# Kernel tuning notes

Measured on AMD Instinct MI355X. Metric: run time of the kernel, lower is better.

The kernel has to match this reference:

```python
import jax, jax.numpy as jnp
import numpy as np

DIM = 1024
NUM_HEADS = 16
HEAD_DIM = DIM // NUM_HEADS


def setup_inputs() -> dict:
    key = jax.random.key(0)
    ks = jax.random.split(key, 8)
    B, N = 4, 1024
    x = jax.random.normal(ks[0], (B, N, DIM), dtype=jnp.float32)
    # RoPE tables per position, broadcast over batch/heads
    pos = jnp.arange(N, dtype=jnp.float32)[:, None]
    inv_freq = 1.0 / (10000.0 ** (jnp.arange(0, HEAD_DIM, 2, dtype=jnp.float32) / HEAD_DIM))
    ang = pos * inv_freq[None, :]                      # [N, D/2]
    ang = jnp.concatenate([ang, ang], axis=-1)          # [N, D]
    cos, sin = jnp.cos(ang), jnp.sin(ang)
    s_in = 1.0 / np.sqrt(DIM)
    qkv_w = jax.random.normal(ks[1], (3 * DIM, DIM), dtype=jnp.float32) * s_in
    qkv_b = jax.random.normal(ks[2], (3 * DIM,), dtype=jnp.float32) * 0.02
    proj_w = jax.random.normal(ks[3], (DIM, DIM), dtype=jnp.float32) * s_in
    proj_b = jax.random.normal(ks[4], (DIM,), dtype=jnp.float32) * 0.02
    return {"x": x, "cos": cos, "sin": sin, "qkv_w": qkv_w, "qkv_b": qkv_b,
            "proj_w": proj_w, "proj_b": proj_b}


def _rotate_half(t):
    t1, t2 = jnp.split(t, 2, axis=-1)
    return jnp.concatenate([-t2, t1], axis=-1)


def reference(x, cos, sin, qkv_w, qkv_b, proj_w, proj_b):
    B, N, C = x.shape
    H, D = NUM_HEADS, HEAD_DIM
    scale = D ** -0.5
    qkv = x @ qkv_w.T + qkv_b                           # [B, N, 3C]
    qkv = qkv.reshape(B, N, 3, H, D).transpose(2, 0, 3, 1, 4)  # [3, B, H, N, D]
    q, k, v = qkv[0], qkv[1], qkv[2]
    q = q * cos + _rotate_half(q) * sin                 # cos/sin [N, D] broadcast
    k = k * cos + _rotate_half(k) * sin
    attn = jnp.einsum('bhnd,bhmd->bhnm', q, k) * scale  # [B, H, N, N]
    attn = jax.nn.softmax(attn, axis=-1)
    out = jnp.einsum('bhnm,bhmd->bhnd', attn, v)        # [B, H, N, D]
    out = out.transpose(0, 2, 1, 3).reshape(B, N, C)
    return out @ proj_w.T + proj_b
```

## Files before the change

### kernel.cpp

```cpp
#include <hip/hip_runtime.h>

typedef __attribute__((ext_vector_type(8))) short bf16x8;
typedef __attribute__((ext_vector_type(4))) float f32x4;
typedef __attribute__((ext_vector_type(4))) unsigned short us4;

#define LOG2E 1.44269504088896f
#define GP(p) (const __attribute__((address_space(1))) void*)(p)
#define LP(p) (__attribute__((address_space(3))) void*)(p)

__device__ inline unsigned short f2bf(float f) {
    unsigned u = __float_as_uint(f);
    u += 0x7fffu + ((u >> 16) & 1u);
    return (unsigned short)(u >> 16);
}

__device__ inline unsigned cvt_pk_bf16(float lo, float hi) {
    unsigned r;
    asm("v_cvt_pk_bf16_f32 %0, %1, %2" : "=v"(r) : "v"(lo), "v"(hi));
    return r;
}

__global__ void cvt_kernel(const float* __restrict__ src, unsigned short* __restrict__ dst, int n) {
    int i = (blockIdx.x * blockDim.x + threadIdx.x) * 4;
    const int stride = gridDim.x * blockDim.x * 4;
    for (; i < n; i += stride) {
        const float4 v = *reinterpret_cast<const float4*>(src + i);
        us4 o;
        o.x = f2bf(v.x); o.y = f2bf(v.y); o.z = f2bf(v.z); o.w = f2bf(v.w);
        *reinterpret_cast<us4*>(dst + i) = o;
    }
}

__device__ inline void gemm_mainloop_db(const unsigned short* __restrict__ A,
                                        const unsigned short* __restrict__ Bw,
                                        unsigned short* As, unsigned short* Bs,
                                        int tm, int tn, f32x4 (&acc)[4][4]) {
    const int K = 1024;
    const int tid = threadIdx.x;
    const int lane = tid & 63;
    const int wv = tid >> 6;
    const int wr = wv >> 1, wc = wv & 1;
    const int lr = lane & 15, lg = lane >> 4;

    const int c1 = tid, c2 = tid + 256;
    const int r1 = c1 >> 2, r2 = c2 >> 2;
    const int g1 = ((c1 & 3) ^ ((r1 >> 1) & 3)) * 8;
    const int g2 = ((c2 & 3) ^ ((r2 >> 1) & 3)) * 8;
    const unsigned short* Ag1 = A + (size_t)(tm * 128 + r1) * K + g1;
    const unsigned short* Ag2 = A + (size_t)(tm * 128 + r2) * K + g2;
    const unsigned short* Bg1 = Bw + (size_t)(tn * 128 + r1) * K + g1;
    const unsigned short* Bg2 = Bw + (size_t)(tn * 128 + r2) * K + g2;

    const int rs = (lr >> 1) & 3;
    const int rdA = (wr * 64 + lr) * 32 + ((0 ^ rs) * 8);
    const int rdB = (wc * 64 + lr) * 32;

    auto STAGE = [&](int buf, int k0) {
        __builtin_amdgcn_global_load_lds(GP(Ag1 + k0), LP(As + buf * 4096 + c1 * 8), 16, 0, 0);
        __builtin_amdgcn_global_load_lds(GP(Ag2 + k0), LP(As + buf * 4096 + c2 * 8), 16, 0, 0);
        __builtin_amdgcn_global_load_lds(GP(Bg1 + k0), LP(Bs + buf * 4096 + c1 * 8), 16, 0, 0);
        __builtin_amdgcn_global_load_lds(GP(Bg2 + k0), LP(Bs + buf * 4096 + c2 * 8), 16, 0, 0);
    };

    STAGE(0, 0);
    for (int t = 0; t < 32; t++) {
        const int buf = t & 1;
        if (t < 31) {
            STAGE(buf ^ 1, (t + 1) * 32);
            asm volatile("s_waitcnt vmcnt(4)" ::: "memory");
        } else {
            asm volatile("s_waitcnt vmcnt(0)" ::: "memory");
        }
        __builtin_amdgcn_s_barrier();
        __builtin_amdgcn_sched_barrier(0);

        bf16x8 af[4], bfv[4];
#pragma unroll
        for (int i = 0; i < 4; i++) {
            const int sl = (lg ^ rs) * 8;
            af[i]  = *reinterpret_cast<const bf16x8*>(As + buf * 4096 + (wr * 64 + i * 16 + lr) * 32 + sl);
            bfv[i] = *reinterpret_cast<const bf16x8*>(Bs + buf * 4096 + (wc * 64 + i * 16 + lr) * 32 + sl);
        }
        __builtin_amdgcn_s_setprio(1);
#pragma unroll
        for (int i = 0; i < 4; i++)
#pragma unroll
            for (int j = 0; j < 4; j++)
                acc[i][j] = __builtin_amdgcn_mfma_f32_16x16x32_bf16(af[i], bfv[j], acc[i][j], 0, 0, 0);
        __builtin_amdgcn_s_setprio(0);
        __builtin_amdgcn_s_barrier();
        __builtin_amdgcn_sched_barrier(0);
    }
}

__global__ __launch_bounds__(256, 3) void gemm_qkv_kernel(
        const unsigned short* __restrict__ A, const unsigned short* __restrict__ Bw,
        const float* __restrict__ bias, const float* __restrict__ cosT, const float* __restrict__ sinT,
        unsigned short* __restrict__ Qb, unsigned short* __restrict__ Kb, unsigned short* __restrict__ Vt) {
    __shared__ __align__(16) unsigned short As[2 * 4096];
    __shared__ __align__(16) unsigned short Bs[2 * 4096];
    const int tid = threadIdx.x;
    const int lane = tid & 63;
    const int wv = tid >> 6;
    const int wr = wv >> 1, wc = wv & 1;
    const int tm = blockIdx.y, tn = blockIdx.x;
    const int lr = lane & 15, lg = lane >> 4;

    f32x4 acc[4][4];
#pragma unroll
    for (int i = 0; i < 4; i++)
#pragma unroll
        for (int j = 0; j < 4; j++)
#pragma unroll
            for (int q = 0; q < 4; q++) acc[i][j][q] = 0.f;

    gemm_mainloop_db(A, Bw, As, Bs, tm, tn, acc);

    const int cbase = tn * 128 + wc * 64;
    const int sec = cbase >> 10;
    const int h = (cbase & 1023) >> 6;
    float bias_c[4];
#pragma unroll
    for (int j = 0; j < 4; j++) bias_c[j] = bias[cbase + j * 16 + lr];

    if (sec == 2) {
#pragma unroll
        for (int i = 0; i < 4; i++) {
            const int m0 = tm * 128 + wr * 64 + i * 16 + lg * 4;
            const int b = m0 >> 10, n0 = m0 & 1023;
#pragma unroll
            for (int j = 0; j < 4; j++) {
                const int d = j * 16 + lr;
                us4 pk;
                pk.x = f2bf(acc[i][j][0] + bias_c[j]); pk.y = f2bf(acc[i][j][1] + bias_c[j]);
                pk.z = f2bf(acc[i][j][2] + bias_c[j]); pk.w = f2bf(acc[i][j][3] + bias_c[j]);
                *reinterpret_cast<us4*>(Vt + ((size_t)((b * 16 + h) * 64 + d)) * 1024 + n0) = pk;
            }
        }
    } else {
#pragma unroll
        for (int i = 0; i < 4; i++) {
#pragma unroll
            for (int r = 0; r < 4; r++) {
                const int m = tm * 128 + wr * 64 + i * 16 + lg * 4 + r;
                const int b = m >> 10, n = m & 1023;
                float vals[4];
#pragma unroll
                for (int j = 0; j < 4; j++) vals[j] = acc[i][j][r] + bias_c[j];
#pragma unroll
                for (int j = 0; j < 4; j++) {
                    const int d = j * 16 + lr;
                    const float c = cosT[n * 64 + d];
                    const float s = sinT[n * 64 + d];
                    const float pr = vals[j ^ 2];
                    float outv = vals[j] * c + (d < 32 ? -pr : pr) * s;
                    if (sec == 0) outv *= 0.125f * LOG2E;
                    unsigned short* dst = (sec == 0) ? Qb : Kb;
                    dst[((size_t)((b * 16 + h) * 1024 + n)) * 64 + d] = f2bf(outv);
                }
            }
        }
    }
}

__global__ __launch_bounds__(256, 4) void attn_kernel(
        const unsigned short* __restrict__ Qb, const unsigned short* __restrict__ Kb,
        const unsigned short* __restrict__ Vt, unsigned short* __restrict__ AO) {
    __shared__ __align__(16) unsigned short KVs[2][8192];
    const int tid = threadIdx.x, lane = tid & 63, wv = tid >> 6;
    const int bh = blockIdx.x, qt = blockIdx.y;
    const int qbase = qt * 64 + wv * 16;
    const unsigned short* Qp = Qb + (size_t)bh * 65536;
    const unsigned short* Kp = Kb + (size_t)bh * 65536;
    const unsigned short* Vp = Vt + (size_t)bh * 65536;
    const int lr = lane & 15, lg = lane >> 4;
    const int koff = (lr >> 2) * 8 + (lr & 3);

    const int s1 = tid, s2 = tid + 256;
    const int r1 = s1 >> 3, r2 = s2 >> 3;
    const int sc1 = (s1 & 7) ^ ((r1 & 3) | ((r1 >> 1) & 4));
    const int sc2 = (s2 & 7) ^ ((r2 & 3) | ((r2 >> 1) & 4));
    const unsigned short* Ks1 = Kp + r1 * 64 + sc1 * 8;
    const unsigned short* Ks2 = Kp + r2 * 64 + sc2 * 8;
    const unsigned short* Vs1 = Vp + r1 * 1024 + sc1 * 8;
    const unsigned short* Vs2 = Vp + r2 * 1024 + sc2 * 8;

    auto STAGE = [&](int buf, int kt) {
        unsigned short* base = &KVs[buf][0];
        __builtin_amdgcn_global_load_lds(GP(Ks1 + kt * 64), LP(base + s1 * 8), 16, 0, 0);
        __builtin_amdgcn_global_load_lds(GP(Ks2 + kt * 64), LP(base + s2 * 8), 16, 0, 0);
        __builtin_amdgcn_global_load_lds(GP(Vs1 + kt), LP(base + 4096 + s1 * 8), 16, 0, 0);
        __builtin_amdgcn_global_load_lds(GP(Vs2 + kt), LP(base + 4096 + s2 * 8), 16, 0, 0);
    };

    bf16x8 qfr[2];
#pragma unroll
    for (int kc = 0; kc < 2; kc++)
        qfr[kc] = *reinterpret_cast<const bf16x8*>(Qp + (qbase + lr) * 64 + kc * 32 + lg * 8);

    f32x4 o[4];
    float m_ = -1e30f, l_ = 0.f;
#pragma unroll
    for (int df = 0; df < 4; df++)
#pragma unroll
        for (int r = 0; r < 4; r++) o[df][r] = 0.f;

    STAGE(0, 0);
    for (int t = 0; t < 16; t++) {
        const int cur = t & 1;
        if (t < 15) {
            STAGE(cur ^ 1, (t + 1) * 64);
            asm volatile("s_waitcnt vmcnt(4)" ::: "memory");
        } else {
            asm volatile("s_waitcnt vmcnt(0)" ::: "memory");
        }
        __builtin_amdgcn_s_barrier();
        __builtin_amdgcn_sched_barrier(0);

        const unsigned short* Kl = &KVs[cur][0];
        const unsigned short* Vl = &KVs[cur][4096];

        f32x4 s[4];
#pragma unroll
        for (int kf = 0; kf < 4; kf++)
#pragma unroll
            for (int r = 0; r < 4; r++) s[kf][r] = 0.f;
        __builtin_amdgcn_s_setprio(1);
#pragma unroll
        for (int kc = 0; kc < 2; kc++) {
#pragma unroll
            for (int kf = 0; kf < 4; kf++) {
                const int row = ((kf >> 1) << 5) + ((kf & 1) << 2) + koff;
                const int col = (kc * 4 + lg) ^ ((row & 3) | ((row >> 1) & 4));
                const bf16x8 kfr = *reinterpret_cast<const bf16x8*>(Kl + row * 64 + col * 8);
                s[kf] = __builtin_amdgcn_mfma_f32_16x16x32_bf16(kfr, qfr[kc], s[kf], 0, 0, 0);
            }
        }
        __builtin_amdgcn_s_setprio(0);

        float mx = s[0][0];
#pragma unroll
        for (int kf = 0; kf < 4; kf++)
#pragma unroll
            for (int r = 0; r < 4; r++) mx = fmaxf(mx, s[kf][r]);
        if (!__all(mx <= m_ + 11.0f)) {
            mx = fmaxf(mx, __shfl_xor(mx, 16, 64));
            mx = fmaxf(mx, __shfl_xor(mx, 32, 64));
            const float mnew = fmaxf(m_, mx);
            const float fsc = exp2f(m_ - mnew);
            m_ = mnew;
            l_ *= fsc;
#pragma unroll
            for (int df = 0; df < 4; df++)
#pragma unroll
                for (int r = 0; r < 4; r++) o[df][r] *= fsc;
        }
        float rs = 0.f;
#pragma unroll
        for (int kf = 0; kf < 4; kf++)
#pragma unroll
            for (int r = 0; r < 4; r++) {
                const float p = exp2f(s[kf][r] - m_);
                s[kf][r] = p;
                rs += p;
            }
        l_ += rs;

#pragma unroll
        for (int kc = 0; kc < 2; kc++) {
            union { bf16x8 v; unsigned u[4]; } pk;
            pk.u[0] = cvt_pk_bf16(s[2 * kc][0], s[2 * kc][1]);
            pk.u[1] = cvt_pk_bf16(s[2 * kc][2], s[2 * kc][3]);
            pk.u[2] = cvt_pk_bf16(s[2 * kc + 1][0], s[2 * kc + 1][1]);
            pk.u[3] = cvt_pk_bf16(s[2 * kc + 1][2], s[2 * kc + 1][3]);
            const bf16x8 pfr = pk.v;
            __builtin_amdgcn_s_setprio(1);
#pragma unroll
            for (int df = 0; df < 4; df++) {
                const int vrow = df * 16 + lr;
                const int vcol = (kc * 4 + lg) ^ ((vrow & 3) | ((vrow >> 1) & 4));
                const bf16x8 vfr = *reinterpret_cast<const bf16x8*>(Vl + vrow * 64 + vcol * 8);
                o[df] = __builtin_amdgcn_mfma_f32_16x16x32_bf16(vfr, pfr, o[df], 0, 0, 0);
            }
            __builtin_amdgcn_s_setprio(0);
        }
        __builtin_amdgcn_s_barrier();
    }

    const int b = bh >> 4, h = bh & 15;
    float lt = l_;
    lt += __shfl_xor(lt, 16, 64);
    lt += __shfl_xor(lt, 32, 64);
    const float rinv = 1.f / lt;
    const int q = qbase + lr;
#pragma unroll
    for (int df = 0; df < 4; df++) {
        us4 pk;
        pk.x = f2bf(o[df][0] * rinv); pk.y = f2bf(o[df][1] * rinv);
        pk.z = f2bf(o[df][2] * rinv); pk.w = f2bf(o[df][3] * rinv);
        *reinterpret_cast<us4*>(AO + (size_t)(b * 1024 + q) * 1024 + h * 64 + df * 16 + lg * 4) = pk;
    }
}

__global__ __launch_bounds__(256, 3) void gemm_proj_kernel(
        const unsigned short* __restrict__ A, const unsigned short* __restrict__ Bw,
        const float* __restrict__ bias, float* __restrict__ out) {
    __shared__ __align__(16) unsigned short As[2 * 4096];
    __shared__ __align__(16) unsigned short Bs[2 * 4096];
    const int tid = threadIdx.x;
    const int lane = tid & 63;
    const int wv = tid >> 6;
    const int wr = wv >> 1, wc = wv & 1;
    const int tm = blockIdx.y, tn = blockIdx.x;
    const int lr = lane & 15, lg = lane >> 4;

    f32x4 acc[4][4];
#pragma unroll
    for (int i = 0; i < 4; i++)
#pragma unroll
        for (int j = 0; j < 4; j++)
#pragma unroll
            for (int q = 0; q < 4; q++) acc[i][j][q] = 0.f;

    gemm_mainloop_db(A, Bw, As, Bs, tm, tn, acc);

#pragma unroll
    for (int i = 0; i < 4; i++)
#pragma unroll
        for (int j = 0; j < 4; j++)
#pragma unroll
            for (int r = 0; r < 4; r++) {
                const int row = tm * 128 + wr * 64 + i * 16 + lg * 4 + r;
                const int col = tn * 128 + wc * 64 + j * 16 + lr;
                out[(size_t)row * 1024 + col] = acc[i][j][r] + bias[col];
            }
}

extern "C" void kernel_launch(void* const* d_in, const int* in_sizes, int n_in,
                              void* d_out, int out_size, void* d_ws, size_t ws_size,
                              hipStream_t stream) {
    const float* x      = (const float*)d_in[0];
    const float* cosT   = (const float*)d_in[1];
    const float* sinT   = (const float*)d_in[2];
    const float* qkv_w  = (const float*)d_in[3];
    const float* qkv_b  = (const float*)d_in[4];
    const float* proj_w = (const float*)d_in[5];
    const float* proj_b = (const float*)d_in[6];
    float* out = (float*)d_out;

    char* ws = (char*)d_ws;
    unsigned short* xb    = (unsigned short*)(ws);
    unsigned short* wqkv  = (unsigned short*)(ws + (8u << 20));
    unsigned short* wproj = (unsigned short*)(ws + (14u << 20));
    unsigned short* Qb    = (unsigned short*)(ws + (16u << 20));
    unsigned short* Kb    = (unsigned short*)(ws + (24u << 20));
    unsigned short* Vt    = (unsigned short*)(ws + (32u << 20));
    unsigned short* AO    = (unsigned short*)(ws + (40u << 20));

    cvt_kernel<<<2048, 256, 0, stream>>>(x, xb, 4096 * 1024);
    cvt_kernel<<<2048, 256, 0, stream>>>(qkv_w, wqkv, 3072 * 1024);
    cvt_kernel<<<1024, 256, 0, stream>>>(proj_w, wproj, 1024 * 1024);
    gemm_qkv_kernel<<<dim3(24, 32), 256, 0, stream>>>(xb, wqkv, qkv_b, cosT, sinT, Qb, Kb, Vt);
    attn_kernel<<<dim3(64, 16), 256, 0, stream>>>(Qb, Kb, Vt, AO);
    gemm_proj_kernel<<<dim3(8, 32), 256, 0, stream>>>(AO, wproj, proj_b, out);
}
```

Measured before the change: 108.3 us.

## Fuse conversion kernels, software-pipeline attention QK/PV, deepen proj GEMM K tile

Merges the three fp32-to-bf16 conversion launches into one kernel that indexes across all three buffers, removing two launches. The attention loop is restructured into a two-stage software pipeline, so the QK^T MFMAs for the next KV tile are issued alongside the PV MFMAs for the current tile, overlapping softmax latency with matrix work. The projection GEMM gets its own mainloop with a 64-wide K tile (double the LDS, occupancy bound lowered from 3 to 2) and half as many barrier iterations. The price is more register and LDS pressure and lower occupancy in the projection kernel.

```diff
diff --git a/kernel.cpp b/kernel.cpp
--- a/kernel.cpp
+++ b/kernel.cpp
@@ -20,14 +20,20 @@
     return r;
 }
 
-__global__ void cvt_kernel(const float* __restrict__ src, unsigned short* __restrict__ dst, int n) {
-    int i = (blockIdx.x * blockDim.x + threadIdx.x) * 4;
-    const int stride = gridDim.x * blockDim.x * 4;
-    for (; i < n; i += stride) {
-        const float4 v = *reinterpret_cast<const float4*>(src + i);
+__global__ void cvt3_kernel(const float* __restrict__ x, const float* __restrict__ qw,
+                            const float* __restrict__ pw,
+                            unsigned short* __restrict__ xb, unsigned short* __restrict__ wqkv,
+                            unsigned short* __restrict__ wproj) {
+    const int nthreads = gridDim.x * blockDim.x;
+    for (int i = blockIdx.x * blockDim.x + threadIdx.x; i < 2097152; i += nthreads) {
+        const float* src; unsigned short* dst; int off;
+        if (i < 1048576)      { src = x;  dst = xb;    off = i; }
+        else if (i < 1835008) { src = qw; dst = wqkv;  off = i - 1048576; }
+        else                  { src = pw; dst = wproj; off = i - 1835008; }
+        const float4 v = *reinterpret_cast<const float4*>(src + off * 4);
         us4 o;
         o.x = f2bf(v.x); o.y = f2bf(v.y); o.z = f2bf(v.z); o.w = f2bf(v.w);
-        *reinterpret_cast<us4*>(dst + i) = o;
+        *reinterpret_cast<us4*>(dst + off * 4) = o;
     }
 }
 
@@ -52,8 +58,6 @@
     const unsigned short* Bg2 = Bw + (size_t)(tn * 128 + r2) * K + g2;
 
     const int rs = (lr >> 1) & 3;
-    const int rdA = (wr * 64 + lr) * 32 + ((0 ^ rs) * 8);
-    const int rdB = (wc * 64 + lr) * 32;
 
     auto STAGE = [&](int buf, int k0) {
         __builtin_amdgcn_global_load_lds(GP(Ag1 + k0), LP(As + buf * 4096 + c1 * 8), 16, 0, 0);
@@ -205,22 +209,7 @@
 #pragma unroll
         for (int r = 0; r < 4; r++) o[df][r] = 0.f;
 
-    STAGE(0, 0);
-    for (int t = 0; t < 16; t++) {
-        const int cur = t & 1;
-        if (t < 15) {
-            STAGE(cur ^ 1, (t + 1) * 64);
-            asm volatile("s_waitcnt vmcnt(4)" ::: "memory");
-        } else {
-            asm volatile("s_waitcnt vmcnt(0)" ::: "memory");
-        }
-        __builtin_amdgcn_s_barrier();
-        __builtin_amdgcn_sched_barrier(0);
-
-        const unsigned short* Kl = &KVs[cur][0];
-        const unsigned short* Vl = &KVs[cur][4096];
-
-        f32x4 s[4];
+    auto QK = [&](f32x4 (&s)[4], const unsigned short* Kl) {
 #pragma unroll
         for (int kf = 0; kf < 4; kf++)
 #pragma unroll
@@ -237,7 +226,9 @@
             }
         }
         __builtin_amdgcn_s_setprio(0);
-
+    };
+
+    auto SMpack = [&](f32x4 (&s)[4], bf16x8 (&pfr)[2]) {
         float mx = s[0][0];
 #pragma unroll
         for (int kf = 0; kf < 4; kf++)
@@ -265,7 +256,6 @@
                 rs += p;
             }
         l_ += rs;
-
 #pragma unroll
         for (int kc = 0; kc < 2; kc++) {
             union { bf16x8 v; unsigned u[4]; } pk;
@@ -273,18 +263,53 @@
             pk.u[1] = cvt_pk_bf16(s[2 * kc][2], s[2 * kc][3]);
             pk.u[2] = cvt_pk_bf16(s[2 * kc + 1][0], s[2 * kc + 1][1]);
             pk.u[3] = cvt_pk_bf16(s[2 * kc + 1][2], s[2 * kc + 1][3]);
-            const bf16x8 pfr = pk.v;
-            __builtin_amdgcn_s_setprio(1);
+            pfr[kc] = pk.v;
+        }
+    };
+
+    auto PV = [&](const unsigned short* Vl, bf16x8 (&pfr)[2]) {
+        __builtin_amdgcn_s_setprio(1);
+#pragma unroll
+        for (int kc = 0; kc < 2; kc++) {
 #pragma unroll
             for (int df = 0; df < 4; df++) {
                 const int vrow = df * 16 + lr;
                 const int vcol = (kc * 4 + lg) ^ ((vrow & 3) | ((vrow >> 1) & 4));
                 const bf16x8 vfr = *reinterpret_cast<const bf16x8*>(Vl + vrow * 64 + vcol * 8);
-                o[df] = __builtin_amdgcn_mfma_f32_16x16x32_bf16(vfr, pfr, o[df], 0, 0, 0);
-            }
-            __builtin_amdgcn_s_setprio(0);
-        }
-        __builtin_amdgcn_s_barrier();
+                o[df] = __builtin_amdgcn_mfma_f32_16x16x32_bf16(vfr, pfr[kc], o[df], 0, 0, 0);
+            }
+        }
+        __builtin_amdgcn_s_setprio(0);
+    };
+
+    STAGE(0, 0);
+    STAGE(1, 64);
+    asm volatile("s_waitcnt vmcnt(4)" ::: "memory");
+    __builtin_amdgcn_s_barrier();
+    __builtin_amdgcn_sched_barrier(0);
+    f32x4 sA[4], sB[4];
+    QK(sA, &KVs[0][0]);
+
+    bf16x8 pfr[2];
+    for (int tt = 0; tt < 8; tt++) {
+        SMpack(sA, pfr);
+        asm volatile("s_waitcnt vmcnt(0)" ::: "memory");
+        __builtin_amdgcn_s_barrier();
+        __builtin_amdgcn_sched_barrier(0);
+        QK(sB, &KVs[1][0]);
+        PV(&KVs[0][4096], pfr);
+        __builtin_amdgcn_s_barrier();
+        __builtin_amdgcn_sched_barrier(0);
+        if (tt < 7) STAGE(0, (2 * tt + 2) * 64);
+        SMpack(sB, pfr);
+        asm volatile("s_waitcnt vmcnt(0)" ::: "memory");
+        __builtin_amdgcn_s_barrier();
+        __builtin_amdgcn_sched_barrier(0);
+        if (tt < 7) QK(sA, &KVs[0][0]);
+        PV(&KVs[1][4096], pfr);
+        __builtin_amdgcn_s_barrier();
+        __builtin_amdgcn_sched_barrier(0);
+        if (tt < 7) STAGE(1, (2 * tt + 3) * 64);
     }
 
     const int b = bh >> 4, h = bh & 15;
@@ -302,11 +327,11 @@
     }
 }
 
-__global__ __launch_bounds__(256, 3) void gemm_proj_kernel(
+__global__ __launch_bounds__(256, 2) void gemm_proj_kernel(
         const unsigned short* __restrict__ A, const unsigned short* __restrict__ Bw,
         const float* __restrict__ bias, float* __restrict__ out) {
-    __shared__ __align__(16) unsigned short As[2 * 4096];
-    __shared__ __align__(16) unsigned short Bs[2 * 4096];
+    __shared__ __align__(16) unsigned short As[2 * 8192];
+    __shared__ __align__(16) unsigned short Bs[2 * 8192];
     const int tid = threadIdx.x;
     const int lane = tid & 63;
     const int wv = tid >> 6;
@@ -314,6 +339,19 @@
     const int tm = blockIdx.y, tn = blockIdx.x;
     const int lr = lane & 15, lg = lane >> 4;
 
+    const unsigned short* Ag[4];
+    const unsigned short* Bg[4];
+    int doff[4];
+#pragma unroll
+    for (int j = 0; j < 4; j++) {
+        const int c = tid + j * 256;
+        const int row = c >> 3, sl = c & 7;
+        const int gs = (sl ^ ((row & 3) | ((row >> 1) & 4))) * 8;
+        Ag[j] = A + (size_t)(tm * 128 + row) * 1024 + gs;
+        Bg[j] = Bw + (size_t)(tn * 128 + row) * 1024 + gs;
+        doff[j] = c * 8;
+    }
+
     f32x4 acc[4][4];
 #pragma unroll
     for (int i = 0; i < 4; i++)
@@ -322,7 +360,51 @@
 #pragma unroll
             for (int q = 0; q < 4; q++) acc[i][j][q] = 0.f;
 
-    gemm_mainloop_db(A, Bw, As, Bs, tm, tn, acc);
+    auto STAGE = [&](int buf, int k0) {
+#pragma unroll
+        for (int j = 0; j < 4; j++)
+            __builtin_amdgcn_global_load_lds(GP(Ag[j] + k0), LP(As + buf * 8192 + doff[j]), 16, 0, 0);
+#pragma unroll
+        for (int j = 0; j < 4; j++)
+            __builtin_amdgcn_global_load_lds(GP(Bg[j] + k0), LP(Bs + buf * 8192 + doff[j]), 16, 0, 0);
+    };
+
+    STAGE(0, 0);
+    for (int t = 0; t < 16; t++) {
+        const int buf = t & 1;
+        if (t < 15) {
+            STAGE(buf ^ 1, (t + 1) * 64);
+            asm volatile("s_waitcnt vmcnt(8)" ::: "memory");
+        } else {
+            asm volatile("s_waitcnt vmcnt(0)" ::: "memory");
+        }
+        __builtin_amdgcn_s_barrier();
+        __builtin_amdgcn_sched_barrier(0);
+
+        bf16x8 af[4][2], bfv[4][2];
+#pragma unroll
+        for (int i = 0; i < 4; i++)
+#pragma unroll
+            for (int kk = 0; kk < 2; kk++) {
+                const int ra = wr * 64 + i * 16 + lr;
+                const int rb = wc * 64 + i * 16 + lr;
+                af[i][kk]  = *reinterpret_cast<const bf16x8*>(
+                    As + buf * 8192 + ra * 64 + ((kk * 4 + lg) ^ ((ra & 3) | ((ra >> 1) & 4))) * 8);
+                bfv[i][kk] = *reinterpret_cast<const bf16x8*>(
+                    Bs + buf * 8192 + rb * 64 + ((kk * 4 + lg) ^ ((rb & 3) | ((rb >> 1) & 4))) * 8);
+            }
+        __builtin_amdgcn_s_setprio(1);
+#pragma unroll
+        for (int i = 0; i < 4; i++)
+#pragma unroll
+            for (int j = 0; j < 4; j++)
+#pragma unroll
+                for (int kk = 0; kk < 2; kk++)
+                    acc[i][j] = __builtin_amdgcn_mfma_f32_16x16x32_bf16(af[i][kk], bfv[j][kk], acc[i][j], 0, 0, 0);
+        __builtin_amdgcn_s_setprio(0);
+        __builtin_amdgcn_s_barrier();
+        __builtin_amdgcn_sched_barrier(0);
+    }
 
 #pragma unroll
     for (int i = 0; i < 4; i++)
@@ -357,9 +439,7 @@
     unsigned short* Vt    = (unsigned short*)(ws + (32u << 20));
     unsigned short* AO    = (unsigned short*)(ws + (40u << 20));
 
-    cvt_kernel<<<2048, 256, 0, stream>>>(x, xb, 4096 * 1024);
-    cvt_kernel<<<2048, 256, 0, stream>>>(qkv_w, wqkv, 3072 * 1024);
-    cvt_kernel<<<1024, 256, 0, stream>>>(proj_w, wproj, 1024 * 1024);
+    cvt3_kernel<<<2048, 256, 0, stream>>>(x, qkv_w, proj_w, xb, wqkv, wproj);
     gemm_qkv_kernel<<<dim3(24, 32), 256, 0, stream>>>(xb, wqkv, qkv_b, cosT, sinT, Qb, Kb, Vt);
     attn_kernel<<<dim3(64, 16), 256, 0, stream>>>(Qb, Kb, Vt, AO);
     gemm_proj_kernel<<<dim3(8, 32), 256, 0, stream>>>(AO, wproj, proj_b, out);
```

After: 102.0 us. -5.8%, faster.
